# Kernel tuning notes

Hardware: AMD Instinct MI355X
Metric: run time of the kernel (lower is better)

Reference implementation:

```python
import jax, jax.numpy as jnp
import numpy as np

LORA_SCALING = 2.0


def setup_inputs() -> dict:
    key = jax.random.key(0)
    ks = jax.random.split(key, 12)
    B, S, H, F, E, R = 1, 2048, 2048, 8192, 8, 16
    s = 0.02  # small init so lora deltas stay numerically sane
    return {
        "hidden_states": jax.random.normal(ks[0], (B, S, H), jnp.float32),
        "gate_w": jax.random.normal(ks[1], (E, H), jnp.float32) * s,
        "Wg": jax.random.normal(ks[2], (F, H), jnp.float32) * s,
        "Wu": jax.random.normal(ks[3], (F, H), jnp.float32) * s,
        "Wd": jax.random.normal(ks[4], (H, F), jnp.float32) * s,
        "Ag": jax.random.normal(ks[5], (E, R, H), jnp.float32) * s,
        "Bg": jax.random.normal(ks[6], (E, F, R), jnp.float32) * s,
        "Au": jax.random.normal(ks[7], (E, R, H), jnp.float32) * s,
        "Bu": jax.random.normal(ks[8], (E, F, R), jnp.float32) * s,
        "Ad": jax.random.normal(ks[9], (E, R, F), jnp.float32) * s,
        "Bd": jax.random.normal(ks[10], (E, H, R), jnp.float32) * s,
        "top_k": 2,
    }


def reference(hidden_states, gate_w, Wg, Wu, Wd, Ag, Bg, Au, Bu, Ad, Bd, top_k):
    B, S, H = hidden_states.shape
    E = gate_w.shape[0]
    h = hidden_states.reshape(-1, H)  # [T, H]
    # router: softmax -> top-k -> renormalize
    logits = h @ gate_w.T                       # [T, E]
    rw = jax.nn.softmax(logits, axis=-1)
    rw_top, sel = jax.lax.top_k(rw, top_k)      # [T, K]
    rw_top = rw_top / jnp.sum(rw_top, axis=-1, keepdims=True)
    # per-token per-expert combine weight (0 if expert not selected)
    w_te = jnp.zeros((h.shape[0], E), h.dtype).at[
        jnp.arange(h.shape[0])[:, None], sel].add(rw_top)  # [T, E]
    # shared base projections computed once for all experts
    common_gate = h @ Wg.T   # [T, F]
    common_up = h @ Wu.T     # [T, F]
    out = jnp.zeros_like(h)
    for e in range(E):  # small fixed expert count; lora deltas are rank-16
        g = common_gate + LORA_SCALING * ((h @ Ag[e].T) @ Bg[e].T)
        u = common_up + LORA_SCALING * ((h @ Au[e].T) @ Bu[e].T)
        act = jax.nn.silu(g) * u                               # [T, F]
        d = act @ Wd.T + LORA_SCALING * ((act @ Ad[e].T) @ Bd[e].T)  # [T, H]
        out = out + w_te[:, e:e + 1] * d
    return out.reshape(B, S, H)
```

## Files before the change

### kernel.cpp

```cpp
#include <hip/hip_runtime.h>
#include <hip/hip_bf16.h>

typedef __attribute__((ext_vector_type(8))) short v8s;
typedef __attribute__((ext_vector_type(4))) float v4f;
typedef unsigned short u16;

static constexpr int TT = 2048;
static constexpr int HD = 2048;
static constexpr int FD = 8192;
static constexpr int NE = 8;
static constexpr int NR = 16;
static constexpr int NXE = 2*FD;
static constexpr int CU_OFF = FD;
static constexpr int KXD = FD + 512;

__device__ __forceinline__ u16 f2b(float f) {
  union { float f; unsigned u; } v; v.f = f;
  unsigned r = v.u + 0x7FFFu + ((v.u >> 16) & 1u);
  return (u16)(r >> 16);
}
__device__ __forceinline__ float b2f(u16 h) {
  union { unsigned u; float f; } v; v.u = ((unsigned)h) << 16;
  return v.f;
}
__device__ __forceinline__ v8s pack8(v4f a, v4f b) {
  v8s r;
  r[0]=(short)f2b(a.x); r[1]=(short)f2b(a.y); r[2]=(short)f2b(a.z); r[3]=(short)f2b(a.w);
  r[4]=(short)f2b(b.x); r[5]=(short)f2b(b.y); r[6]=(short)f2b(b.z); r[7]=(short)f2b(b.w);
  return r;
}
__device__ __forceinline__ void gload_lds16(const void* g, void* l) {
  __builtin_amdgcn_global_load_lds(
      (const __attribute__((address_space(1))) unsigned int*)g,
      (__attribute__((address_space(3))) unsigned int*)l, 16, 0, 0);
}
__device__ __forceinline__ void barrier_pin() {
  __builtin_amdgcn_s_barrier();
  __builtin_amdgcn_sched_barrier(0);
}
__device__ __forceinline__ void vm_wait4() { asm volatile("s_waitcnt vmcnt(4)" ::: "memory"); }
__device__ __forceinline__ void vm_wait0() { asm volatile("s_waitcnt vmcnt(0)" ::: "memory"); }

template<int Q>
__device__ __forceinline__ void mmq(v4f (&acc)[8][4], const v8s (&af)[2][2], const v8s (&bf)[4][2]) {
  __builtin_amdgcn_s_setprio(1);
  #pragma unroll
  for (int m2 = 0; m2 < 2; ++m2)
    #pragma unroll
    for (int nf = 0; nf < 4; ++nf) {
      acc[Q*2+m2][nf] = __builtin_amdgcn_mfma_f32_16x16x32_bf16(af[m2][0], bf[nf][0], acc[Q*2+m2][nf], 0, 0, 0);
      acc[Q*2+m2][nf] = __builtin_amdgcn_mfma_f32_16x16x32_bf16(af[m2][1], bf[nf][1], acc[Q*2+m2][nf], 0, 0, 0);
    }
  __builtin_amdgcn_s_setprio(0);
}

static constexpr int PREP_BLOCKS = 7424;
__global__ __launch_bounds__(256)
void prep_kernel(const float* __restrict__ h, const float* __restrict__ Wg,
                 const float* __restrict__ Wu, const float* __restrict__ Wd,
                 const float* __restrict__ Ag, const float* __restrict__ Au,
                 const float* __restrict__ Bg, const float* __restrict__ Bu,
                 const float* __restrict__ Ad, const float* __restrict__ Bd,
                 u16* __restrict__ hb, u16* __restrict__ Bgux, u16* __restrict__ Agu,
                 u16* __restrict__ Wdx, u16* __restrict__ Bgb, u16* __restrict__ Bub,
                 u16* __restrict__ Adb, float* __restrict__ hAx) {
  const int b = blockIdx.x, tid = threadIdx.x;
  auto cast32at = [&](const float* s, u16* d) {
    v4f a0 = *(const v4f*)(s),    a1 = *(const v4f*)(s+4);
    v4f a2 = *(const v4f*)(s+8),  a3 = *(const v4f*)(s+12);
    v4f a4 = *(const v4f*)(s+16), a5 = *(const v4f*)(s+20);
    v4f a6 = *(const v4f*)(s+24), a7 = *(const v4f*)(s+28);
    *(v8s*)(d)    = pack8(a0, a1);
    *(v8s*)(d+8)  = pack8(a2, a3);
    *(v8s*)(d+16) = pack8(a4, a5);
    *(v8s*)(d+24) = pack8(a6, a7);
  };
  auto cast32 = [&](const float* s, u16* d, long blk) {
    long i = blk*8192 + (long)tid*32;
    cast32at(s+i, d+i);
  };
  if (b < 512) { cast32(h, hb, b); }
  else if (b < 2560) { cast32(Wg, Bgux, b-512); }
  else if (b < 4608) { cast32(Wu, Bgux + (size_t)FD*HD, b-2560); }
  else if (b < 6656) {
    long idx = (long)(b-4608)*8192 + (long)tid*32;
    long r = idx >> 13; int c = (int)(idx & 8191);
    cast32at(Wd + r*FD + c, Wdx + r*KXD + c);
  }
  else if (b < 6688) { cast32(Ag, Agu, b-6656); }
  else if (b < 6720) { cast32(Au, Agu + (size_t)128*HD, b-6688); }
  else if (b < 6848) { cast32(Bg, Bgb, b-6720); }
  else if (b < 6976) { cast32(Bu, Bub, b-6848); }
  else if (b < 7104) { cast32(Ad, Adb, b-6976); }
  else if (b < 7360) {
    long idx = (long)(b-7104)*4096 + (long)tid*16;
    int hrow = (int)(idx >> 9); int c = (int)(idx & 511);
    u16* d = Wdx + (size_t)hrow*KXD + FD + c;
    if (c < 128) {
      const float* s = Bd + ((size_t)(c>>4)*HD + hrow)*16;
      v4f a0 = *(const v4f*)s,     a1 = *(const v4f*)(s+4);
      v4f a2 = *(const v4f*)(s+8), a3 = *(const v4f*)(s+12);
      *(v8s*)d     = pack8(a0, a1);
      *(v8s*)(d+8) = pack8(a2, a3);
    } else {
      v8s z = {0,0,0,0,0,0,0,0};
      *(v8s*)d = z; *(v8s*)(d+8) = z;
    }
  } else {
    long i = (long)(b-7360)*8192 + (long)tid*32;
    v4f z = {0.f,0.f,0.f,0.f};
    #pragma unroll
    for (int q = 0; q < 8; ++q) *(v4f*)(hAx+i+q*4) = z;
  }
}

__global__ __launch_bounds__(64)
void router_kernel(const float* __restrict__ h, const float* __restrict__ gw,
                   int* __restrict__ sel, int* __restrict__ count,
                   int* __restrict__ listTok, float* __restrict__ listW) {
  int t = blockIdx.x, lane = threadIdx.x;
  const float* hp = h + (size_t)t * HD;
  float acc[8] = {0,0,0,0,0,0,0,0};
  for (int i = lane; i < HD; i += 64) {
    float hv = hp[i];
    #pragma unroll
    for (int e = 0; e < 8; ++e) acc[e] += hv * gw[e*HD + i];
  }
  #pragma unroll
  for (int off = 32; off > 0; off >>= 1) {
    #pragma unroll
    for (int e = 0; e < 8; ++e) acc[e] += __shfl_xor(acc[e], off, 64);
  }
  if (lane == 0) {
    int e0 = -1, e1 = -1; float b0 = -1e30f, b1 = -1e30f;
    #pragma unroll
    for (int e = 0; e < 8; ++e) {
      float v = acc[e];
      if (v > b0) { b1 = b0; e1 = e0; b0 = v; e0 = e; }
      else if (v > b1) { b1 = v; e1 = e; }
    }
    float p1 = __expf(b1 - b0);
    float w0 = 1.f / (1.f + p1);
    float w1 = p1 * w0;
    sel[2*t] = e0; sel[2*t+1] = e1;
    int pos0 = atomicAdd(&count[e0], 1);
    listTok[e0*TT + pos0] = t;           listW[e0*TT + pos0] = w0;
    int pos1 = atomicAdd(&count[e1], 1);
    listTok[e1*TT + pos1] = t | (1<<20); listW[e1*TT + pos1] = w1;
  }
}

__global__ __launch_bounds__(256)
void gemm128a(const u16* __restrict__ A, const u16* __restrict__ B, float* __restrict__ Cout,
              int K, int ldc) {
  __shared__ u16 As[128*64];
  __shared__ u16 Bs[128*64];
  const int tid  = threadIdx.x;
  const int lane = tid & 63, wid = tid >> 6;
  const int gx = gridDim.x;
  const int lin = blockIdx.y * gx + blockIdx.x;
  const int chunk = (gx * gridDim.y) >> 3;
  const int wg = (lin & 7) * chunk + (lin >> 3);
  const int m0 = (wg % gx) * 128, n0 = (wg / gx) * 128;
  const int kc = K / gridDim.z;
  const int kbeg = blockIdx.z * kc;
  const int wr = wid >> 1, wc = wid & 1;
  const int lrow = lane >> 3, lcol = (lane & 7) * 8;
  v4f acc[4][4];
  #pragma unroll
  for (int mi = 0; mi < 4; ++mi)
    #pragma unroll
    for (int ni = 0; ni < 4; ++ni) acc[mi][ni] = (v4f){0.f,0.f,0.f,0.f};

  for (int k0 = kbeg; k0 < kbeg + kc; k0 += 64) {
    #pragma unroll
    for (int it = 0; it < 4; ++it) {
      int seg = wid*4 + it;
      int row = seg*8 + lrow;
      gload_lds16(A + (size_t)(m0+row)*K + k0 + lcol, As + seg*512);
      gload_lds16(B + (size_t)(n0+row)*K + k0 + lcol, Bs + seg*512);
    }
    __syncthreads();
    #pragma unroll
    for (int kk = 0; kk < 64; kk += 32) {
      v8s af[4], bfr[4];
      #pragma unroll
      for (int mi = 0; mi < 4; ++mi)
        af[mi] = *(const v8s*)(As + (wr*64 + mi*16 + (lane&15))*64 + kk + (lane>>4)*8);
      #pragma unroll
      for (int ni = 0; ni < 4; ++ni)
        bfr[ni] = *(const v8s*)(Bs + (wc*64 + ni*16 + (lane&15))*64 + kk + (lane>>4)*8);
      #pragma unroll
      for (int mi = 0; mi < 4; ++mi)
        #pragma unroll
        for (int ni = 0; ni < 4; ++ni)
          acc[mi][ni] = __builtin_amdgcn_mfma_f32_16x16x32_bf16(af[mi], bfr[ni], acc[mi][ni], 0, 0, 0);
    }
    __syncthreads();
  }

  #pragma unroll
  for (int mi = 0; mi < 4; ++mi)
    #pragma unroll
    for (int j = 0; j < 4; ++j) {
      int row = m0 + wr*64 + mi*16 + (lane>>4)*4 + j;
      size_t base = (size_t)row*ldc + n0 + wc*64 + (lane&15);
      #pragma unroll
      for (int ni = 0; ni < 4; ++ni)
        atomicAdd(&Cout[base + ni*16], acc[mi][ni][j]);
    }
}

template<int MODE>
__global__ __launch_bounds__(512, 2)
void gemm256(const u16* __restrict__ A, const u16* __restrict__ B, void* __restrict__ Cout,
             int ldk, int kchunk, int ldc) {
  __shared__ u16 lds[2][2][2][8192];
  const int tid = threadIdx.x, lane = tid & 63, wid = tid >> 6;
  const int gx = gridDim.x;
  const int nwg = gx * gridDim.y;
  const int lin = blockIdx.y * gx + blockIdx.x;
  const int chunk = nwg >> 3;
  const int wg = (lin & 7) * chunk + (lin >> 3);
  const int m0 = (wg % gx) * 256, n0 = (wg / gx) * 256;
  const long kbeg = (long)blockIdx.z * kchunk;
  const int NK = kchunk >> 6, NI = NK >> 1;
  const int wr = wid >> 2, wc = wid & 3;

  const int s_r = (wid << 4) + (lane >> 3);
  const int s_c = lane & 7;

  auto STAGE = [&](int slot, int ab, int half, const u16* M, int rc0, int kt) {
    const u16* g0 = M + (size_t)(rc0 + half*128 + s_r) * ldk + kbeg + kt*64 + ((s_c ^ (s_r & 7)) << 3);
    gload_lds16(g0, &lds[slot][ab][half][wid << 10]);
    const int r1 = s_r + 8;
    const u16* g1 = M + (size_t)(rc0 + half*128 + r1) * ldk + kbeg + kt*64 + ((s_c ^ (r1 & 7)) << 3);
    gload_lds16(g1, &lds[slot][ab][half][(wid << 10) + 512]);
  };
  auto LDA = [&](int slot, int mf, int c16b) -> v8s {
    int rr = (mf << 4) + (lane & 15);
    return *(const v8s*)&lds[slot][0][wr][rr*64 + (((c16b + (lane >> 4)) ^ (rr & 7)) << 3)];
  };
  auto LDB = [&](int slot, int nf, int c16b) -> v8s {
    int row = (wc << 6) + (nf << 4) + (lane & 15);
    int rr = row & 127;
    return *(const v8s*)&lds[slot][1][row >> 7][rr*64 + (((c16b + (lane >> 4)) ^ (rr & 7)) << 3)];
  };

  v4f acc[8][4];
  #pragma unroll
  for (int mf = 0; mf < 8; ++mf)
    #pragma unroll
    for (int nf = 0; nf < 4; ++nf) acc[mf][nf] = (v4f){0.f,0.f,0.f,0.f};

  STAGE(0,1,0,B,n0,0); STAGE(0,1,1,B,n0,0);
  STAGE(0,0,0,A,m0,0); STAGE(0,0,1,A,m0,0);
  STAGE(1,1,0,B,n0,1); STAGE(1,1,1,B,n0,1);
  vm_wait4();
  barrier_pin();

  for (int i = 0; i < NI; ++i) {
    const int kt0 = 2*i, kt1 = kt0 + 1;
    const int kt2c = (kt0 + 2 < NK) ? kt0 + 2 : kt0;
    const bool s45 = (kt0 + 2 < NK), s67 = (kt1 + 2 < NK);
    v8s bf[4][2], af[2][2];
    #pragma unroll
    for (int nf = 0; nf < 4; ++nf) { bf[nf][0] = LDB(0,nf,0); bf[nf][1] = LDB(0,nf,4); }
    af[0][0]=LDA(0,0,0); af[0][1]=LDA(0,0,4); af[1][0]=LDA(0,1,0); af[1][1]=LDA(0,1,4);
    STAGE(1,0,0,A,m0,kt1);
    barrier_pin(); mmq<0>(acc,af,bf); barrier_pin();
    af[0][0]=LDA(0,2,0); af[0][1]=LDA(0,2,4); af[1][0]=LDA(0,3,0); af[1][1]=LDA(0,3,4);
    STAGE(1,0,1,A,m0,kt1);
    barrier_pin(); mmq<1>(acc,af,bf); barrier_pin();
    af[0][0]=LDA(0,4,0); af[0][1]=LDA(0,4,4); af[1][0]=LDA(0,5,0); af[1][1]=LDA(0,5,4);
    STAGE(0,1,0,B,n0,kt2c);
    barrier_pin(); mmq<2>(acc,af,bf); barrier_pin();
    af[0][0]=LDA(0,6,0); af[0][1]=LDA(0,6,4); af[1][0]=LDA(0,7,0); af[1][1]=LDA(0,7,4);
    STAGE(0,1,1,B,n0,kt2c);
    vm_wait4();
    barrier_pin(); mmq<3>(acc,af,bf); barrier_pin();
    #pragma unroll
    for (int nf = 0; nf < 4; ++nf) { bf[nf][0] = LDB(1,nf,0); bf[nf][1] = LDB(1,nf,4); }
    af[0][0]=LDA(1,0,0); af[0][1]=LDA(1,0,4); af[1][0]=LDA(1,1,0); af[1][1]=LDA(1,1,4);
    if (s45) STAGE(0,0,0,A,m0,kt0+2);
    barrier_pin(); mmq<0>(acc,af,bf); barrier_pin();
    af[0][0]=LDA(1,2,0); af[0][1]=LDA(1,2,4); af[1][0]=LDA(1,3,0); af[1][1]=LDA(1,3,4);
    if (s45) STAGE(0,0,1,A,m0,kt0+2);
    barrier_pin(); mmq<1>(acc,af,bf); barrier_pin();
    af[0][0]=LDA(1,4,0); af[0][1]=LDA(1,4,4); af[1][0]=LDA(1,5,0); af[1][1]=LDA(1,5,4);
    if (s67) STAGE(1,1,0,B,n0,kt1+2);
    barrier_pin(); mmq<2>(acc,af,bf); barrier_pin();
    af[0][0]=LDA(1,6,0); af[0][1]=LDA(1,6,4); af[1][0]=LDA(1,7,0); af[1][1]=LDA(1,7,4);
    if (s67) STAGE(1,1,1,B,n0,kt1+2);
    vm_wait4();
    barrier_pin(); mmq<3>(acc,af,bf); barrier_pin();
  }
  vm_wait0();

  if (MODE == 0) {
    u16* C = (u16*)Cout;
    #pragma unroll
    for (int mf = 0; mf < 8; ++mf)
      #pragma unroll
      for (int j = 0; j < 4; ++j) {
        int row = m0 + wr*128 + mf*16 + (lane>>4)*4 + j;
        size_t base = (size_t)row*ldc + n0 + wc*64 + (lane&15);
        #pragma unroll
        for (int nf = 0; nf < 4; ++nf)
          C[base + nf*16] = f2b(acc[mf][nf][j]);
      }
  } else {
    float* C = (float*)Cout + (size_t)blockIdx.z * TT * HD;
    #pragma unroll
    for (int mf = 0; mf < 8; ++mf)
      #pragma unroll
      for (int j = 0; j < 4; ++j) {
        int row = m0 + wr*128 + mf*16 + (lane>>4)*4 + j;
        size_t base = (size_t)row*ldc + n0 + wc*64 + (lane&15);
        #pragma unroll
        for (int nf = 0; nf < 4; ++nf)
          C[base + nf*16] = acc[mf][nf][j];
      }
  }
}

__global__ __launch_bounds__(256)
void reduce4_kernel(const float* __restrict__ P, float* __restrict__ out) {
  long i = ((long)blockIdx.x * 256 + threadIdx.x) * 4;
  const size_t S = (size_t)TT * HD;
  v4f s = *(const v4f*)(P + i);
  s = s + *(const v4f*)(P + S + i);
  s = s + *(const v4f*)(P + 2*S + i);
  s = s + *(const v4f*)(P + 3*S + i);
  *(v4f*)(out + i) = s;
}

static constexpr int HA_LD = 40;
static constexpr int AW_LD = 72;
static constexpr int CT_LD = 72;

struct PF {
  v8s bg[4], bu[4], ad[2];
  v8s rg0, ru0, rg1, ru1;
};

__global__ __launch_bounds__(256)
void expert_kernel(const u16* __restrict__ CGU,
                   const float* __restrict__ hAx,
                   const u16* __restrict__ Bgb, const u16* __restrict__ Bub,
                   const u16* __restrict__ Adb,
                   const int* __restrict__ count, const int* __restrict__ listTok,
                   const float* __restrict__ listW,
                   u16* __restrict__ actw0, u16* __restrict__ actw1,
                   float* __restrict__ cC) {
  const int e = blockIdx.y, g = blockIdx.x, fb = blockIdx.z;
  const int n = count[e];
  if (g*16 >= n) return;
  const int tid = threadIdx.x, lane = tid & 63, w = tid >> 6;
  __shared__ u16 hAg[16*HA_LD], hAu[16*HA_LD];
  __shared__ u16 AWs[4][16*AW_LD];
  __shared__ u16 cgT[4][16*CT_LD], cuT[4][16*CT_LD];
  __shared__ int sTok[16], sSlot[16];
  __shared__ float sW[16];
  __shared__ float dAred[4][256];

  if (tid < 16) {
    int idx = g*16 + tid;
    if (idx < n) {
      int ent = listTok[e*TT + idx];
      sTok[tid] = ent & 0xFFFF; sSlot[tid] = (ent >> 20) & 1; sW[tid] = listW[e*TT + idx];
    } else { sTok[tid] = TT; sSlot[tid] = 0; sW[tid] = 0.f; }
  }
  __syncthreads();
  if (tid < 128) {
    int tensor = tid >> 6;
    int sub = tid & 63;
    int row = sub >> 2, c8 = (sub & 3) * 8;
    int trd = min(sTok[row], TT - 1);
    u16 vals[8];
    if (c8 < 16) {
      const float* src = hAx + (size_t)trd*256 + tensor*128 + e*NR + c8;
      v4f a = *(const v4f*)src, b = *(const v4f*)(src + 4);
      v8s p = pack8(a, b);
      #pragma unroll
      for (int q = 0; q < 8; ++q) vals[q] = (u16)p[q];
    } else {
      #pragma unroll
      for (int q = 0; q < 8; ++q) vals[q] = 0;
    }
    u16* dst = (tensor ? hAu : hAg) + row*HA_LD + c8;
    #pragma unroll
    for (int q = 0; q < 8; ++q) dst[q] = vals[q];
  }
  __syncthreads();

  int tR[4], slR[4]; float wR[4];
  #pragma unroll
  for (int j = 0; j < 4; ++j) {
    int r = (lane>>4)*4 + j;
    tR[j] = sTok[r]; slR[j] = sSlot[r]; wR[j] = sW[r];
  }
  const int khalf = lane >> 4;
  v8s afg = *(const v8s*)(hAg + (lane&15)*HA_LD + khalf*8);
  v8s afu = *(const v8s*)(hAu + (lane&15)*HA_LD + khalf*8);
  v4f accDA = (v4f){0.f,0.f,0.f,0.f};
  u16* aww = AWs[w]; u16* cgw = cgT[w]; u16* cuw = cuT[w];
  const v8s zero8 = {0,0,0,0,0,0,0,0};
  const u16* BgE = Bgb + (size_t)e*FD*16;
  const u16* BuE = Bub + (size_t)e*FD*16;
  const u16* AdE = Adb + (size_t)e*16*FD;

  const int srj = lane >> 2, sc = (lane & 3) * 16;
  const int srow = lane >> 3, c8s = (lane & 7) * 8;
  const size_t trdA = (size_t)min(sTok[srow], TT - 1);
  const size_t trdB = (size_t)min(sTok[srow + 8], TT - 1);

  auto LOADPF = [&](int ch, PF& p) {
    const int f0 = ch * 64;
    #pragma unroll
    for (int nf = 0; nf < 4; ++nf) {
      int f = f0 + nf*16 + (lane & 15);
      p.bg[nf] = (khalf < 2) ? *(const v8s*)(BgE + (size_t)f*16 + khalf*8) : zero8;
      p.bu[nf] = (khalf < 2) ? *(const v8s*)(BuE + (size_t)f*16 + khalf*8) : zero8;
    }
    #pragma unroll
    for (int ks = 0; ks < 2; ++ks)
      p.ad[ks] = *(const v8s*)(AdE + (size_t)(lane&15)*FD + f0 + ks*32 + khalf*8);
    p.rg0 = *(const v8s*)(CGU + trdA*NXE + f0 + c8s);
    p.ru0 = *(const v8s*)(CGU + trdA*NXE + CU_OFF + f0 + c8s);
    p.rg1 = *(const v8s*)(CGU + trdB*NXE + f0 + c8s);
    p.ru1 = *(const v8s*)(CGU + trdB*NXE + CU_OFF + f0 + c8s);
  };

  auto COMPUTE = [&](int ch, const PF& p) {
    const int f0 = ch * 64;
    *(v8s*)(cgw + srow*CT_LD + c8s)     = p.rg0;
    *(v8s*)(cgw + (srow+8)*CT_LD + c8s) = p.rg1;
    *(v8s*)(cuw + srow*CT_LD + c8s)     = p.ru0;
    *(v8s*)(cuw + (srow+8)*CT_LD + c8s) = p.ru1;
    v4f dg[4], du[4];
    #pragma unroll
    for (int nf = 0; nf < 4; ++nf) {
      dg[nf] = __builtin_amdgcn_mfma_f32_16x16x32_bf16(afg, p.bg[nf], (v4f){0.f,0.f,0.f,0.f}, 0, 0, 0);
      du[nf] = __builtin_amdgcn_mfma_f32_16x16x32_bf16(afu, p.bu[nf], (v4f){0.f,0.f,0.f,0.f}, 0, 0, 0);
    }
    #pragma unroll
    for (int nf = 0; nf < 4; ++nf) {
      #pragma unroll
      for (int j = 0; j < 4; ++j) {
        int rj = (lane>>4)*4 + j;
        int fi = nf*16 + (lane&15);
        float cgv = b2f(cgw[rj*CT_LD + fi]);
        float cuv = b2f(cuw[rj*CT_LD + fi]);
        float gv = cgv + 2.f * dg[nf][j];
        float uv = cuv + 2.f * du[nf][j];
        float a  = gv * __builtin_amdgcn_rcpf(1.f + __expf(-gv)) * uv;
        aww[rj*AW_LD + fi] = f2b(wR[j] * a);
      }
    }
    {
      int st = sTok[srj], ss = sSlot[srj];
      u16* dst = (ss ? actw1 : actw0) + (size_t)st*FD + f0 + sc;
      *(v8s*)dst       = *(const v8s*)(aww + srj*AW_LD + sc);
      *(v8s*)(dst + 8) = *(const v8s*)(aww + srj*AW_LD + sc + 8);
    }
    #pragma unroll
    for (int ks = 0; ks < 2; ++ks) {
      v8s aA = *(const v8s*)(aww + (lane&15)*AW_LD + ks*32 + khalf*8);
      accDA = __builtin_amdgcn_mfma_f32_16x16x32_bf16(aA, p.ad[ks], accDA, 0, 0, 0);
    }
  };

  const int ch0 = fb*16 + w;
  PF pA, pB;
  LOADPF(ch0,      pA);
  LOADPF(ch0 + 4,  pB);
  COMPUTE(ch0,     pA);
  LOADPF(ch0 + 8,  pA);
  COMPUTE(ch0 + 4, pB);
  LOADPF(ch0 + 12, pB);
  COMPUTE(ch0 + 8, pA);
  COMPUTE(ch0 + 12, pB);

  #pragma unroll
  for (int j = 0; j < 4; ++j)
    dAred[w][((lane>>4)*4 + j)*16 + (lane&15)] = accDA[j];
  __syncthreads();
  {
    int row = tid >> 4, col = tid & 15;
    float s2 = dAred[0][row*16+col] + dAred[1][row*16+col] + dAred[2][row*16+col] + dAred[3][row*16+col];
    atomicAdd(&cC[((size_t)sTok[row]*2 + sSlot[row])*16 + col], 2.f * s2);
  }
}

__global__ __launch_bounds__(256)
void combine2_kernel(const u16* __restrict__ a0, const u16* __restrict__ a1,
                     const float* __restrict__ cC, const int* __restrict__ sel,
                     u16* __restrict__ abx) {
  int t = blockIdx.x, tid = threadIdx.x;
  const u16* p0 = a0 + (size_t)t * FD;
  const u16* p1 = a1 + (size_t)t * FD;
  u16* po = abx + (size_t)t * KXD;
  for (int i = tid * 8; i < FD; i += 256 * 8) {
    v8s x = *(const v8s*)(p0 + i);
    v8s y = *(const v8s*)(p1 + i);
    v8s o;
    #pragma unroll
    for (int j = 0; j < 8; ++j) o[j] = (short)f2b(b2f((u16)x[j]) + b2f((u16)y[j]));
    *(v8s*)(po + i) = o;
  }
  for (int c = tid; c < 512; c += 256) {
    float v = 0.f;
    if (c < 128) {
      int e_i = c >> 4, r = c & 15;
      if (sel[2*t]     == e_i) v += cC[((size_t)t*2 + 0)*16 + r];
      if (sel[2*t + 1] == e_i) v += cC[((size_t)t*2 + 1)*16 + r];
    }
    po[FD + c] = f2b(v);
  }
}

extern "C" void kernel_launch(void* const* d_in, const int* in_sizes, int n_in,
                              void* d_out, int out_size, void* d_ws, size_t ws_size,
                              hipStream_t stream) {
  (void)in_sizes; (void)n_in; (void)out_size; (void)ws_size;
  const float* h  = (const float*)d_in[0];
  const float* gw = (const float*)d_in[1];
  const float* Wg = (const float*)d_in[2];
  const float* Wu = (const float*)d_in[3];
  const float* Wd = (const float*)d_in[4];
  const float* Ag = (const float*)d_in[5];
  const float* Bg = (const float*)d_in[6];
  const float* Au = (const float*)d_in[7];
  const float* Bu = (const float*)d_in[8];
  const float* Ad = (const float*)d_in[9];
  const float* Bd = (const float*)d_in[10];

  char* ws = (char*)d_ws;
  size_t off = 0;
  auto alloc = [&](size_t bytes) { size_t c = off; off += (bytes + 255) & ~(size_t)255; return c; };
  u16*  hb     = (u16*)(ws + alloc((size_t)TT*HD*2));
  u16*  Bgux   = (u16*)(ws + alloc((size_t)(TT+1)*FD*2*2));
  u16*  Agu    = (u16*)(ws + alloc((size_t)256*HD*2));
  u16*  Wdx    = (u16*)(ws + alloc((size_t)HD*KXD*2));
  u16*  CGU    = (u16*)(ws + alloc((size_t)TT*NXE*2));
  u16*  Bgb    = (u16*)(ws + alloc((size_t)NE*FD*16*2));
  u16*  Bub    = (u16*)(ws + alloc((size_t)NE*FD*16*2));
  u16*  Adb    = (u16*)(ws + alloc((size_t)NE*16*FD*2));
  float* hAx   = (float*)(ws + alloc((size_t)TT*256*4));
  float* cC    = (float*)(ws + alloc((size_t)(TT+1)*2*16*4));
  int*  sel    = (int*)(ws + alloc((size_t)TT*2*4));
  int*  count  = (int*)(ws + alloc(256));
  int*  listTok= (int*)(ws + alloc((size_t)NE*TT*4));
  float* listW = (float*)(ws + alloc((size_t)NE*TT*4));
  u16*  actw0  = Bgux;
  u16*  actw1  = Bgux + (size_t)(TT+1)*FD;
  u16*  abx    = CGU;
  float* parts = (float*)Bgux;

  hipMemsetAsync(count, 0, NE*sizeof(int), stream);
  hipMemsetAsync(cC, 0, (size_t)(TT+1)*2*16*4, stream);

  prep_kernel<<<PREP_BLOCKS, 256, 0, stream>>>(h, Wg, Wu, Wd, Ag, Au, Bg, Bu, Ad, Bd,
                                               hb, Bgux, Agu, Wdx, Bgb, Bub, Adb, hAx);

  router_kernel<<<TT, 64, 0, stream>>>(h, gw, sel, count, listTok, listW);

  gemm128a<<<dim3(16, 2, 8), 256, 0, stream>>>(hb, Agu, hAx, HD, 256);

  gemm256<0><<<dim3(8, 32, 1), 512, 0, stream>>>(hb, Bgux, CGU, HD, HD, NXE);
  gemm256<0><<<dim3(8, 32, 1), 512, 0, stream>>>(hb, Bgux + (size_t)FD*HD, CGU + CU_OFF, HD, HD, NXE);

  expert_kernel<<<dim3(128, NE, 8), 256, 0, stream>>>(CGU, hAx, Bgb, Bub, Adb, count, listTok, listW,
                                                      actw0, actw1, cC);

  combine2_kernel<<<TT, 256, 0, stream>>>(actw0, actw1, cC, sel, abx);

  gemm256<3><<<dim3(8, 8, 4), 512, 0, stream>>>(abx, Wdx, parts, KXD, KXD/4, HD);

  reduce4_kernel<<<4096, 256, 0, stream>>>(parts, (float*)d_out);
}
```

Baseline: 453.7 us.

## Fuse router into prep kernel, merge memsets and gate/up GEMM launches

Moves the router computation into the prep kernel as additional virtual blocks, processed by a grid-stride loop over half-size cast chunks. The two memsets are merged into one by placing count right after cC. The gate and up projection GEMMs become a single launch with a doubled grid. Weight cast stores to Wdx use nontemporal stores. The aim is fewer launches and better overlap of the small router work with bandwidth-bound casting, at the cost of a heavier prep kernel.

Measured after the change: 436.6 us. 3.8% less time.

```diff
diff --git a/kernel.cpp b/kernel.cpp
--- a/kernel.cpp
+++ b/kernel.cpp
@@ -54,99 +54,103 @@
   __builtin_amdgcn_s_setprio(0);
 }
 
-static constexpr int PREP_BLOCKS = 7424;
+static constexpr int PREP_VB = 15104;
+static constexpr int PREP_BLOCKS = 7552;
 __global__ __launch_bounds__(256)
 void prep_kernel(const float* __restrict__ h, const float* __restrict__ Wg,
                  const float* __restrict__ Wu, const float* __restrict__ Wd,
                  const float* __restrict__ Ag, const float* __restrict__ Au,
                  const float* __restrict__ Bg, const float* __restrict__ Bu,
                  const float* __restrict__ Ad, const float* __restrict__ Bd,
+                 const float* __restrict__ gw,
                  u16* __restrict__ hb, u16* __restrict__ Bgux, u16* __restrict__ Agu,
                  u16* __restrict__ Wdx, u16* __restrict__ Bgb, u16* __restrict__ Bub,
-                 u16* __restrict__ Adb, float* __restrict__ hAx) {
-  const int b = blockIdx.x, tid = threadIdx.x;
-  auto cast32at = [&](const float* s, u16* d) {
-    v4f a0 = *(const v4f*)(s),    a1 = *(const v4f*)(s+4);
-    v4f a2 = *(const v4f*)(s+8),  a3 = *(const v4f*)(s+12);
-    v4f a4 = *(const v4f*)(s+16), a5 = *(const v4f*)(s+20);
-    v4f a6 = *(const v4f*)(s+24), a7 = *(const v4f*)(s+28);
-    *(v8s*)(d)    = pack8(a0, a1);
-    *(v8s*)(d+8)  = pack8(a2, a3);
-    *(v8s*)(d+16) = pack8(a4, a5);
-    *(v8s*)(d+24) = pack8(a6, a7);
-  };
-  auto cast32 = [&](const float* s, u16* d, long blk) {
-    long i = blk*8192 + (long)tid*32;
-    cast32at(s+i, d+i);
-  };
-  if (b < 512) { cast32(h, hb, b); }
-  else if (b < 2560) { cast32(Wg, Bgux, b-512); }
-  else if (b < 4608) { cast32(Wu, Bgux + (size_t)FD*HD, b-2560); }
-  else if (b < 6656) {
-    long idx = (long)(b-4608)*8192 + (long)tid*32;
-    long r = idx >> 13; int c = (int)(idx & 8191);
-    cast32at(Wd + r*FD + c, Wdx + r*KXD + c);
-  }
-  else if (b < 6688) { cast32(Ag, Agu, b-6656); }
-  else if (b < 6720) { cast32(Au, Agu + (size_t)128*HD, b-6688); }
-  else if (b < 6848) { cast32(Bg, Bgb, b-6720); }
-  else if (b < 6976) { cast32(Bu, Bub, b-6848); }
-  else if (b < 7104) { cast32(Ad, Adb, b-6976); }
-  else if (b < 7360) {
-    long idx = (long)(b-7104)*4096 + (long)tid*16;
-    int hrow = (int)(idx >> 9); int c = (int)(idx & 511);
-    u16* d = Wdx + (size_t)hrow*KXD + FD + c;
-    if (c < 128) {
-      const float* s = Bd + ((size_t)(c>>4)*HD + hrow)*16;
+                 u16* __restrict__ Adb, float* __restrict__ hAx,
+                 int* __restrict__ sel, int* __restrict__ count,
+                 int* __restrict__ listTok, float* __restrict__ listW) {
+  const int tid = threadIdx.x;
+  for (int vb = blockIdx.x; vb < PREP_VB; vb += PREP_BLOCKS) {
+    const int b = vb;
+    auto cast16 = [&](const float* s, u16* d, long blk) {
+      long i = blk*4096 + (long)tid*16;
+      v4f a0 = *(const v4f*)(s+i),    a1 = *(const v4f*)(s+i+4);
+      v4f a2 = *(const v4f*)(s+i+8),  a3 = *(const v4f*)(s+i+12);
+      *(v8s*)(d+i)   = pack8(a0, a1);
+      *(v8s*)(d+i+8) = pack8(a2, a3);
+    };
+    if (b < 1024) { cast16(h, hb, b); }
+    else if (b < 5120)  { cast16(Wg, Bgux, b-1024); }
+    else if (b < 9216)  { cast16(Wu, Bgux + (size_t)FD*HD, b-5120); }
+    else if (b < 13312) {
+      long idx = (long)(b-9216)*4096 + (long)tid*16;
+      long r = idx >> 13; int c = (int)(idx & 8191);
+      const float* s = Wd + r*FD + c;
+      u16* d = Wdx + r*KXD + c;
       v4f a0 = *(const v4f*)s,     a1 = *(const v4f*)(s+4);
       v4f a2 = *(const v4f*)(s+8), a3 = *(const v4f*)(s+12);
-      *(v8s*)d     = pack8(a0, a1);
-      *(v8s*)(d+8) = pack8(a2, a3);
-    } else {
-      v8s z = {0,0,0,0,0,0,0,0};
-      *(v8s*)d = z; *(v8s*)(d+8) = z;
-    }
-  } else {
-    long i = (long)(b-7360)*8192 + (long)tid*32;
-    v4f z = {0.f,0.f,0.f,0.f};
-    #pragma unroll
-    for (int q = 0; q < 8; ++q) *(v4f*)(hAx+i+q*4) = z;
-  }
-}
-
-__global__ __launch_bounds__(64)
-void router_kernel(const float* __restrict__ h, const float* __restrict__ gw,
-                   int* __restrict__ sel, int* __restrict__ count,
-                   int* __restrict__ listTok, float* __restrict__ listW) {
-  int t = blockIdx.x, lane = threadIdx.x;
-  const float* hp = h + (size_t)t * HD;
-  float acc[8] = {0,0,0,0,0,0,0,0};
-  for (int i = lane; i < HD; i += 64) {
-    float hv = hp[i];
-    #pragma unroll
-    for (int e = 0; e < 8; ++e) acc[e] += hv * gw[e*HD + i];
-  }
-  #pragma unroll
-  for (int off = 32; off > 0; off >>= 1) {
-    #pragma unroll
-    for (int e = 0; e < 8; ++e) acc[e] += __shfl_xor(acc[e], off, 64);
-  }
-  if (lane == 0) {
-    int e0 = -1, e1 = -1; float b0 = -1e30f, b1 = -1e30f;
-    #pragma unroll
-    for (int e = 0; e < 8; ++e) {
-      float v = acc[e];
-      if (v > b0) { b1 = b0; e1 = e0; b0 = v; e0 = e; }
-      else if (v > b1) { b1 = v; e1 = e; }
-    }
-    float p1 = __expf(b1 - b0);
-    float w0 = 1.f / (1.f + p1);
-    float w1 = p1 * w0;
-    sel[2*t] = e0; sel[2*t+1] = e1;
-    int pos0 = atomicAdd(&count[e0], 1);
-    listTok[e0*TT + pos0] = t;           listW[e0*TT + pos0] = w0;
-    int pos1 = atomicAdd(&count[e1], 1);
-    listTok[e1*TT + pos1] = t | (1<<20); listW[e1*TT + pos1] = w1;
+      __builtin_nontemporal_store(pack8(a0, a1), (v8s*)d);
+      __builtin_nontemporal_store(pack8(a2, a3), (v8s*)(d+8));
+    }
+    else if (b < 13376) { cast16(Ag, Agu, b-13312); }
+    else if (b < 13440) { cast16(Au, Agu + (size_t)128*HD, b-13376); }
+    else if (b < 13696) { cast16(Bg, Bgb, b-13440); }
+    else if (b < 13952) { cast16(Bu, Bub, b-13696); }
+    else if (b < 14208) { cast16(Ad, Adb, b-13952); }
+    else if (b < 14464) {
+      long idx = (long)(b-14208)*4096 + (long)tid*16;
+      int hrow = (int)(idx >> 9); int c = (int)(idx & 511);
+      u16* d = Wdx + (size_t)hrow*KXD + FD + c;
+      if (c < 128) {
+        const float* s = Bd + ((size_t)(c>>4)*HD + hrow)*16;
+        v4f a0 = *(const v4f*)s,     a1 = *(const v4f*)(s+4);
+        v4f a2 = *(const v4f*)(s+8), a3 = *(const v4f*)(s+12);
+        __builtin_nontemporal_store(pack8(a0, a1), (v8s*)d);
+        __builtin_nontemporal_store(pack8(a2, a3), (v8s*)(d+8));
+      } else {
+        v8s z = {0,0,0,0,0,0,0,0};
+        __builtin_nontemporal_store(z, (v8s*)d);
+        __builtin_nontemporal_store(z, (v8s*)(d+8));
+      }
+    }
+    else if (b < 14592) {
+      long i = (long)(b-14464)*4096 + (long)tid*16;
+      v4f z = {0.f,0.f,0.f,0.f};
+      *(v4f*)(hAx+i) = z; *(v4f*)(hAx+i+4) = z;
+      *(v4f*)(hAx+i+8) = z; *(v4f*)(hAx+i+12) = z;
+    }
+    else {
+      int t = (b - 14592)*4 + (tid >> 6);
+      int lane = tid & 63;
+      const float* hp = h + (size_t)t * HD;
+      float acc[8] = {0,0,0,0,0,0,0,0};
+      for (int i = lane; i < HD; i += 64) {
+        float hv = hp[i];
+        #pragma unroll
+        for (int e = 0; e < 8; ++e) acc[e] += hv * gw[e*HD + i];
+      }
+      #pragma unroll
+      for (int off = 32; off > 0; off >>= 1) {
+        #pragma unroll
+        for (int e = 0; e < 8; ++e) acc[e] += __shfl_xor(acc[e], off, 64);
+      }
+      if (lane == 0) {
+        int e0 = -1, e1 = -1; float b0 = -1e30f, b1 = -1e30f;
+        #pragma unroll
+        for (int e = 0; e < 8; ++e) {
+          float v = acc[e];
+          if (v > b0) { b1 = b0; e1 = e0; b0 = v; e0 = e; }
+          else if (v > b1) { b1 = v; e1 = e; }
+        }
+        float p1 = __expf(b1 - b0);
+        float w0 = 1.f / (1.f + p1);
+        float w1 = p1 * w0;
+        sel[2*t] = e0; sel[2*t+1] = e1;
+        int pos0 = atomicAdd(&count[e0], 1);
+        listTok[e0*TT + pos0] = t;           listW[e0*TT + pos0] = w0;
+        int pos1 = atomicAdd(&count[e1], 1);
+        listTok[e1*TT + pos1] = t | (1<<20); listW[e1*TT + pos1] = w1;
+      }
+    }
   }
 }
 
@@ -548,9 +552,10 @@
   u16*  Bub    = (u16*)(ws + alloc((size_t)NE*FD*16*2));
   u16*  Adb    = (u16*)(ws + alloc((size_t)NE*16*FD*2));
   float* hAx   = (float*)(ws + alloc((size_t)TT*256*4));
+  size_t cC_bytes = ((size_t)(TT+1)*2*16*4 + 255) & ~(size_t)255;
   float* cC    = (float*)(ws + alloc((size_t)(TT+1)*2*16*4));
+  int*  count  = (int*)(ws + alloc(256));
   int*  sel    = (int*)(ws + alloc((size_t)TT*2*4));
-  int*  count  = (int*)(ws + alloc(256));
   int*  listTok= (int*)(ws + alloc((size_t)NE*TT*4));
   float* listW = (float*)(ws + alloc((size_t)NE*TT*4));
   u16*  actw0  = Bgux;
@@ -558,18 +563,15 @@
   u16*  abx    = CGU;
   float* parts = (float*)Bgux;
 
-  hipMemsetAsync(count, 0, NE*sizeof(int), stream);
-  hipMemsetAsync(cC, 0, (size_t)(TT+1)*2*16*4, stream);
-
-  prep_kernel<<<PREP_BLOCKS, 256, 0, stream>>>(h, Wg, Wu, Wd, Ag, Au, Bg, Bu, Ad, Bd,
-                                               hb, Bgux, Agu, Wdx, Bgb, Bub, Adb, hAx);
-
-  router_kernel<<<TT, 64, 0, stream>>>(h, gw, sel, count, listTok, listW);
+  hipMemsetAsync(cC, 0, cC_bytes + 256, stream);
+
+  prep_kernel<<<PREP_BLOCKS, 256, 0, stream>>>(h, Wg, Wu, Wd, Ag, Au, Bg, Bu, Ad, Bd, gw,
+                                               hb, Bgux, Agu, Wdx, Bgb, Bub, Adb, hAx,
+                                               sel, count, listTok, listW);
 
   gemm128a<<<dim3(16, 2, 8), 256, 0, stream>>>(hb, Agu, hAx, HD, 256);
 
-  gemm256<0><<<dim3(8, 32, 1), 512, 0, stream>>>(hb, Bgux, CGU, HD, HD, NXE);
-  gemm256<0><<<dim3(8, 32, 1), 512, 0, stream>>>(hb, Bgux + (size_t)FD*HD, CGU + CU_OFF, HD, HD, NXE);
+  gemm256<0><<<dim3(8, 64, 1), 512, 0, stream>>>(hb, Bgux, CGU, HD, HD, NXE);
 
   expert_kernel<<<dim3(128, NE, 8), 256, 0, stream>>>(CGU, hAx, Bgb, Bub, Adb, count, listTok, listW,
                                                       actw0, actw1, cC);
```
